# Kernel optimization log

Hardware: AMD Instinct MI355X
Metric: run time of the kernel (lower is better)

The kernel has to match this reference:

```python
import jax, jax.numpy as jnp
import numpy as np
import math

T_SCALE = 99
FEAT_DIM = 400
BATCH = 2
C = 256
NH = 8
NS = 32
NSPB = 3
RATIO = 0.5
LOCAL_STEP = 33


def build_sample_mask(T=T_SCALE, ns=NS, nspb=NSPB, ratio=RATIO):
    # Vectorized port of _get_interp1d_mask. Flat layout: [time, (bin, start, end)].
    N = ns * nspb
    e_idx, s_idx = np.meshgrid(np.arange(T), np.arange(T), indexing='ij')
    valid = s_idx < e_idx
    starts_i = s_idx[valid].astype(np.int64)
    ends_i = e_idx[valid].astype(np.int64)
    starts = starts_i.astype(np.float64)
    ends = ends_i.astype(np.float64)
    center = ends - starts + 1.0
    xmin = starts - center * ratio
    plen = (ends + center * ratio) - xmin
    S = xmin[:, None] + (plen / (N - 1.0))[:, None] * np.arange(N)[None, :]  # [P, N]
    down = np.trunc(S).astype(np.int64)  # matches int(math.modf(s)[1]) (trunc toward 0)
    dec = S - down                       # can be negative when s < 0, as in the original
    up = np.ceil(S).astype(np.int64)
    bin_col = (np.arange(N) // nspb)[None, :] * (T * T) + (starts_i * T + ends_i)[:, None]
    M = np.zeros(T * ns * T * T, np.float64)
    vd = (down >= 0) & (down <= T - 1)
    np.add.at(M, (down * (ns * T * T) + bin_col)[vd], ((1.0 - dec) / nspb)[vd])
    vu = (up >= 0) & (up <= T - 1)
    np.add.at(M, (up * (ns * T * T) + bin_col)[vu], (dec / nspb)[vu])
    return M.reshape(T, ns * T * T).astype(np.float32)


def pos_ebb(scale, size):
    pos = jnp.arange(scale, dtype=jnp.float32)[:, None]
    div = jnp.exp(jnp.arange(0, size, 2, dtype=jnp.float32) * (-math.log(10000.0) / size))
    ang = pos * div
    # interleave sin (even) / cos (odd)
    return jnp.stack([jnp.sin(ang), jnp.cos(ang)], axis=-1).reshape(scale, size)


def layer_norm(x, g, b, eps=1e-5):
    mu = jnp.mean(x, -1, keepdims=True)
    var = jnp.mean((x - mu) ** 2, -1, keepdims=True)
    return (x - mu) * jax.lax.rsqrt(var + eps) * g + b


def mha(x, w_qkv, b_qkv, w_o, b_o, nh=NH):
    t, b, c = x.shape
    hd = c // nh
    q, k, v = jnp.split(x @ w_qkv.T + b_qkv, 3, axis=-1)
    q = q.reshape(t, b, nh, hd)
    k = k.reshape(t, b, nh, hd)
    v = v.reshape(t, b, nh, hd)
    att = jnp.einsum('qbhd,kbhd->bhqk', q, k) / math.sqrt(hd)
    att = jax.nn.softmax(att, axis=-1)
    o = jnp.einsum('bhqk,kbhd->qbhd', att, v).reshape(t, b, c)
    return o @ w_o.T + b_o


def encoder(x, p):
    # PyTorch post-norm TransformerEncoder (eval mode, dropout off) + final LayerNorm
    (qkv_w, qkv_b, o_w, o_b, l1_w, l1_b, l2_w, l2_b, n1_g, n1_b, n2_g, n2_b, nf_g, nf_b) = p
    for i in range(qkv_w.shape[0]):
        a = mha(x, qkv_w[i], qkv_b[i], o_w[i], o_b[i])
        x = layer_norm(x + a, n1_g[i], n1_b[i])
        f = jax.nn.relu(x @ l1_w[i].T + l1_b[i]) @ l2_w[i].T + l2_b[i]
        x = layer_norm(x + f, n2_g[i], n2_b[i])
    return layer_norm(x, nf_g, nf_b)


def conv1d(x, w, b, pad, groups=1):
    y = jax.lax.conv_general_dilated(x, w, (1,), [(pad, pad)],
                                     dimension_numbers=('NCH', 'OIH', 'NCH'),
                                     feature_group_count=groups)
    return y + b[None, :, None]


def conv2d(x, w, b, pad):
    y = jax.lax.conv_general_dilated(x, w, (1, 1), [(pad, pad), (pad, pad)],
                                     dimension_numbers=('NCHW', 'OIHW', 'NCHW'))
    return y + b[None, :, None, None]


def conv3d(x, w, b, stride):
    y = jax.lax.conv_general_dilated(x, w, stride, [(0, 0)] * 3,
                                     dimension_numbers=('NCDHW', 'OIDHW', 'NCDHW'))
    return y + b[None, :, None, None, None]


def _forward(x, cb_w, cb_b, tg_qkv_w, tg_qkv_b, tg_o_w, tg_o_b, tg_l1_w, tg_l1_b, tg_l2_w, tg_l2_b, tg_n1_g, tg_n1_b, tg_n2_g, tg_n2_b, tg_nf_g, tg_nf_b, tl_qkv_w, tl_qkv_b, tl_o_w, tl_o_b, tl_l1_w, tl_l1_b, tl_l2_w, tl_l2_b, tl_n1_g, tl_n1_b, tl_n2_g, tl_n2_b, tl_nf_g, tl_nf_b, s1_w, s1_b, s2_w, s2_b, c3_w, c3_b, p1_w, p1_b, p2_w, p2_b, p3_w, p3_b, sample_mask):
    B, _, T = x.shape
    base = jax.nn.relu(conv1d(x, cb_w, cb_b, pad=1, groups=4))  # [B,C,T]
    # local transformer on LOCAL_STEP-strided windows
    group = T // LOCAL_STEP
    tl_p = (tl_qkv_w, tl_qkv_b, tl_o_w, tl_o_b, tl_l1_w, tl_l1_b, tl_l2_w, tl_l2_b, tl_n1_g, tl_n1_b, tl_n2_g, tl_n2_b, tl_nf_g, tl_nf_b)
    feat = base.reshape(B, C, LOCAL_STEP, group).transpose(2, 3, 0, 1).reshape(LOCAL_STEP, B * group, C)
    feat = encoder(feat + pos_ebb(LOCAL_STEP, C)[:, None, :], tl_p)
    local = feat.reshape(LOCAL_STEP * group, B, C).transpose(1, 2, 0)  # [B,C,T]
    # global bidirectional transformer (shared weights, flipped second pass)
    tg_p = (tg_qkv_w, tg_qkv_b, tg_o_w, tg_o_b, tg_l1_w, tg_l1_b, tg_l2_w, tg_l2_b, tg_n1_g, tg_n1_b, tg_n2_g, tg_n2_b, tg_nf_g, tg_nf_b)
    g = base.transpose(2, 0, 1)  # [T,B,C]
    pe = pos_ebb(T, C)[:, None, :]
    f1 = encoder(g + pe, tg_p)
    f2 = encoder(g[::-1] + pe, tg_p)
    base2 = local + (f1 + f2[::-1]).transpose(1, 2, 0)  # [B,C,T]
    s = jax.nn.relu(conv1d(base2, s1_w, s1_b, pad=1, groups=4))
    start1 = jax.nn.sigmoid(conv1d(s, s2_w, s2_b, pad=0))[:, 0, :]  # [B,T]
    # boundary-matching layer: dense matmul against precomputed interp mask
    bm = jnp.matmul(base2, sample_mask).reshape(B, C, NS, T, T)
    p = jax.nn.relu(conv3d(bm, c3_w, c3_b, (NS, 1, 1)))[:, :, 0]  # [B,C,T,T]
    p = jax.nn.relu(conv2d(p, p1_w, p1_b, pad=1))
    p = jax.nn.relu(conv2d(p, p2_w, p2_b, pad=1))
    cm = jax.nn.sigmoid(conv2d(p, p3_w, p3_b, pad=0))  # [B,2,T,T]
    return cm, start1


def setup_inputs() -> dict:
    key = jax.random.key(0)
    ks = iter(jax.random.split(key, 80))
    def rnd(shape):
        return 0.02 * jax.random.normal(next(ks), shape, dtype=jnp.float32)
    inp = {'x': jax.random.normal(next(ks), (BATCH, FEAT_DIM, T_SCALE), dtype=jnp.float32)}
    inp['cb_w'] = rnd((C, FEAT_DIM // 4, 3)); inp['cb_b'] = jnp.zeros((C,), jnp.float32)
    for pre, n in (('tg', 6), ('tl', 3)):
        inp[pre + '_qkv_w'] = rnd((n, 3 * C, C)); inp[pre + '_qkv_b'] = jnp.zeros((n, 3 * C), jnp.float32)
        inp[pre + '_o_w'] = rnd((n, C, C)); inp[pre + '_o_b'] = jnp.zeros((n, C), jnp.float32)
        inp[pre + '_l1_w'] = rnd((n, 1024, C)); inp[pre + '_l1_b'] = jnp.zeros((n, 1024), jnp.float32)
        inp[pre + '_l2_w'] = rnd((n, C, 1024)); inp[pre + '_l2_b'] = jnp.zeros((n, C), jnp.float32)
        inp[pre + '_n1_g'] = jnp.ones((n, C), jnp.float32); inp[pre + '_n1_b'] = jnp.zeros((n, C), jnp.float32)
        inp[pre + '_n2_g'] = jnp.ones((n, C), jnp.float32); inp[pre + '_n2_b'] = jnp.zeros((n, C), jnp.float32)
        inp[pre + '_nf_g'] = jnp.ones((C,), jnp.float32); inp[pre + '_nf_b'] = jnp.zeros((C,), jnp.float32)
    inp['s1_w'] = rnd((C, C // 4, 3)); inp['s1_b'] = jnp.zeros((C,), jnp.float32)
    inp['s2_w'] = rnd((1, C, 1)); inp['s2_b'] = jnp.zeros((1,), jnp.float32)
    inp['c3_w'] = rnd((C, C, NS, 1, 1)); inp['c3_b'] = jnp.zeros((C,), jnp.float32)
    inp['p1_w'] = rnd((C, C, 3, 3)); inp['p1_b'] = jnp.zeros((C,), jnp.float32)
    inp['p2_w'] = rnd((C, C, 3, 3)); inp['p2_b'] = jnp.zeros((C,), jnp.float32)
    inp['p3_w'] = rnd((2, C, 1, 1)); inp['p3_b'] = jnp.zeros((2,), jnp.float32)
    inp['sample_mask'] = jnp.asarray(build_sample_mask())  # [T, NS*T*T], exact BMN interp mask
    return inp


def reference(x, cb_w, cb_b, tg_qkv_w, tg_qkv_b, tg_o_w, tg_o_b, tg_l1_w, tg_l1_b, tg_l2_w, tg_l2_b, tg_n1_g, tg_n1_b, tg_n2_g, tg_n2_b, tg_nf_g, tg_nf_b, tl_qkv_w, tl_qkv_b, tl_o_w, tl_o_b, tl_l1_w, tl_l1_b, tl_l2_w, tl_l2_b, tl_n1_g, tl_n1_b, tl_n2_g, tl_n2_b, tl_nf_g, tl_nf_b, s1_w, s1_b, s2_w, s2_b, c3_w, c3_b, p1_w, p1_b, p2_w, p2_b, p3_w, p3_b, sample_mask):
    return _forward(x, cb_w, cb_b, tg_qkv_w, tg_qkv_b, tg_o_w, tg_o_b, tg_l1_w, tg_l1_b, tg_l2_w, tg_l2_b, tg_n1_g, tg_n1_b, tg_n2_g, tg_n2_b, tg_nf_g, tg_nf_b, tl_qkv_w, tl_qkv_b, tl_o_w, tl_o_b, tl_l1_w, tl_l1_b, tl_l2_w, tl_l2_b, tl_n1_g, tl_n1_b, tl_n2_g, tl_n2_b, tl_nf_g, tl_nf_b, s1_w, s1_b, s2_w, s2_b, c3_w, c3_b, p1_w, p1_b, p2_w, p2_b, p3_w, p3_b, sample_mask)
```

## Files before the change

kernel.cpp:

```cpp
#include <hip/hip_runtime.h>
#include <math.h>

#define T99   99
#define CC    256
#define NHH   8
#define FEAT  400
#define NS_   32
#define LSTEP 33

typedef __attribute__((ext_vector_type(8))) short s8v;
typedef __attribute__((ext_vector_type(4))) float f4v;

__device__ __forceinline__ void mfma_bf16(f4v& d, s8v a, s8v b) {
  asm volatile("v_mfma_f32_16x16x32_bf16 %0, %1, %2, %0" : "+v"(d) : "v"(a), "v"(b));
}

__device__ __forceinline__ unsigned short f2bf(float f) {
  union { float f; unsigned u; } x; x.f = f;
  unsigned r = x.u + 0x7FFFu + ((x.u >> 16) & 1u);
  return (unsigned short)(r >> 16);
}
__device__ __forceinline__ float bf2f(unsigned short h) {
  union { unsigned u; float f; } x; x.u = ((unsigned)h) << 16;
  return x.f;
}
__device__ __forceinline__ float blo(unsigned u) { union { unsigned x; float f; } c; c.x = u << 16; return c.f; }
__device__ __forceinline__ float bhi(unsigned u) { union { unsigned x; float f; } c; c.x = u & 0xffff0000u; return c.f; }

__device__ __forceinline__ float pe_val(int pos, int c) {
  int i = c >> 1;
  float freq = expf((float)(2 * i) * (-0.03597789207803197f));
  float ang = (float)pos * freq;
  return (c & 1) ? cosf(ang) : sinf(ang);
}

__global__ __launch_bounds__(128) void k_convbase(const float* __restrict__ x,
                                                  const float* __restrict__ w,
                                                  const float* __restrict__ bias,
                                                  float* __restrict__ base) {
  int b = blockIdx.x >> 8, co = blockIdx.x & 255, t = threadIdx.x;
  if (t >= T99) return;
  int g = co >> 6;
  float acc = bias[co];
  const float* xp = x + (size_t)(b * FEAT + g * 100) * T99;
  const float* wp = w + (size_t)co * 300;
  for (int ic = 0; ic < 100; ++ic) {
    float x0 = (t > 0)  ? xp[ic * T99 + t - 1] : 0.f;
    float x1 = xp[ic * T99 + t];
    float x2 = (t < 98) ? xp[ic * T99 + t + 1] : 0.f;
    acc += wp[ic * 3] * x0 + wp[ic * 3 + 1] * x1 + wp[ic * 3 + 2] * x2;
  }
  base[(size_t)(b * CC + co) * T99 + t] = fmaxf(acc, 0.f);
}

__global__ __launch_bounds__(256) void k_convW(const float* __restrict__ qkv, const float* __restrict__ o,
                                               const float* __restrict__ l1, const float* __restrict__ l2,
                                               int L, unsigned short* __restrict__ dst) {
  int total = L * 786432;
  for (int idx = blockIdx.x * 256 + threadIdx.x; idx < total; idx += gridDim.x * 256) {
    int l = idx / 786432, r = idx % 786432;
    float v;
    if (r < 196608)      v = qkv[(size_t)l * 196608 + r];
    else if (r < 262144) v = o[(size_t)l * 65536 + (r - 196608)];
    else if (r < 524288) v = l1[(size_t)l * 262144 + (r - 262144)];
    else                 v = l2[(size_t)l * 262144 + (r - 524288)];
    dst[idx] = f2bf(v);
  }
}

__global__ __launch_bounds__(256) void k_build_xg(const float* __restrict__ base, float* __restrict__ xg,
                                                  unsigned short* __restrict__ xgb) {
  int idx = blockIdx.x * 256 + threadIdx.x;
  int t = idx >> 10, r = idx & 1023, b4 = r >> 8, c = r & 255;
  float v = (b4 < 2) ? base[(size_t)(b4 * CC + c) * T99 + t]
                     : base[(size_t)((b4 - 2) * CC + c) * T99 + (98 - t)];
  v += pe_val(t, c);
  xg[idx] = v; xgb[idx] = f2bf(v);
}

__global__ __launch_bounds__(256) void k_build_xl(const float* __restrict__ base, float* __restrict__ xl,
                                                  unsigned short* __restrict__ xlb) {
  int idx = blockIdx.x * 256 + threadIdx.x;
  int ls = idx / 1536, r = idx % 1536, j = r >> 8, c = r & 255;
  int g = j >> 1, b = j & 1, t = ls * 3 + g;
  float v = base[(size_t)(b * CC + c) * T99 + t] + pe_val(ls, c);
  xl[idx] = v; xlb[idx] = f2bf(v);
}

__device__ __forceinline__ void gemm_body(const unsigned short* __restrict__ A,
                                          const unsigned short* __restrict__ W,
                                          const float* __restrict__ bias,
                                          const float* __restrict__ R,
                                          float* __restrict__ Y,
                                          unsigned short* __restrict__ Yb,
                                          int M, int N, int K, int flags,
                                          int m0, int n0) {
  __shared__ __align__(16) unsigned short Al[64][40];
  __shared__ __align__(16) unsigned short Bl[64][40];
  int tid = threadIdx.x;
  int lane = tid & 63, w = tid >> 6, wm = w >> 1, wn = w & 1;
  int sp = tid >> 2, kc = (tid & 3) << 3;
  f4v zero4 = {0.f, 0.f, 0.f, 0.f};
  f4v acc[2][2];
#pragma unroll
  for (int mt = 0; mt < 2; ++mt)
#pragma unroll
    for (int nt = 0; nt < 2; ++nt) acc[mt][nt] = zero4;

  for (int k0 = 0; k0 < K; k0 += 32) {
    s8v av = {0, 0, 0, 0, 0, 0, 0, 0};
    int row = m0 + sp;
    if (row < M) av = *(const s8v*)&A[(size_t)row * K + k0 + kc];
    *(s8v*)&Al[sp][kc] = av;
    *(s8v*)&Bl[sp][kc] = *(const s8v*)&W[(size_t)(n0 + sp) * K + k0 + kc];
    __syncthreads();
    s8v af[2], bf[2];
#pragma unroll
    for (int mt = 0; mt < 2; ++mt)
      af[mt] = *(const s8v*)&Al[wm * 32 + mt * 16 + (lane & 15)][(lane >> 4) * 8];
#pragma unroll
    for (int nt = 0; nt < 2; ++nt)
      bf[nt] = *(const s8v*)&Bl[wn * 32 + nt * 16 + (lane & 15)][(lane >> 4) * 8];
#pragma unroll
    for (int mt = 0; mt < 2; ++mt)
#pragma unroll
      for (int nt = 0; nt < 2; ++nt) mfma_bf16(acc[mt][nt], af[mt], bf[nt]);
    __syncthreads();
  }
  asm volatile("s_nop 7\n\ts_nop 7\n\ts_nop 4");
#pragma unroll
  for (int mt = 0; mt < 2; ++mt) {
#pragma unroll
    for (int nt = 0; nt < 2; ++nt) {
      int col = n0 + wn * 32 + nt * 16 + (lane & 15);
      float bv = bias[col];
#pragma unroll
      for (int r = 0; r < 2 * 2; ++r) {
        int row = m0 + wm * 32 + mt * 16 + (lane >> 4) * 4 + r;
        if (row < M) {
          float v = acc[mt][nt][r] + bv;
          if (flags & 2) v += R[(size_t)row * N + col];
          if (flags & 1) v = fmaxf(v, 0.f);
          if (!(flags & 8)) Y[(size_t)row * N + col] = v;
          if (flags & 4) Yb[(size_t)row * N + col] = f2bf(v);
        }
      }
    }
  }
}

__global__ __launch_bounds__(256) void k_gemmb(const unsigned short* __restrict__ A,
                                               const unsigned short* __restrict__ W,
                                               const float* __restrict__ bias,
                                               const float* __restrict__ R,
                                               float* __restrict__ Y,
                                               unsigned short* __restrict__ Yb,
                                               int M, int N, int K, int flags) {
  gemm_body(A, W, bias, R, Y, Yb, M, N, K, flags, blockIdx.x * 64, blockIdx.y * 64);
}

__global__ __launch_bounds__(256) void k_gemmb2(const unsigned short* __restrict__ A0,
                                                const unsigned short* __restrict__ W0,
                                                const float* __restrict__ bias0,
                                                const float* __restrict__ R0,
                                                float* __restrict__ Y0,
                                                unsigned short* __restrict__ Yb0,
                                                int M0,
                                                const unsigned short* __restrict__ A1,
                                                const unsigned short* __restrict__ W1,
                                                const float* __restrict__ bias1,
                                                const float* __restrict__ R1,
                                                float* __restrict__ Y1,
                                                unsigned short* __restrict__ Yb1,
                                                int M1,
                                                int N, int K, int flags) {
  int m0 = blockIdx.x * 64;
  if (blockIdx.z == 0) {
    if (m0 >= M0) return;
    gemm_body(A0, W0, bias0, R0, Y0, Yb0, M0, N, K, flags, m0, blockIdx.y * 64);
  } else {
    if (m0 >= M1) return;
    gemm_body(A1, W1, bias1, R1, Y1, Yb1, M1, N, K, flags, m0, blockIdx.y * 64);
  }
}

__device__ __forceinline__ void attn_body(const unsigned short* __restrict__ qkv,
                                          unsigned short* __restrict__ attb,
                                          int T_, int B_, int bid) {
  __shared__ float qv[32];
  __shared__ float red[128];
  __shared__ float pv[128];
  int tid = threadIdx.x;
  int q = bid % T_;
  int h = (bid / T_) % NHH;
  int b = bid / (T_ * NHH);
  if (tid < 32) qv[tid] = bf2f(qkv[(size_t)(q * B_ + b) * 768 + h * 32 + tid]);
  __syncthreads();
  float s = -1e30f;
  if (tid < T_) {
    const unsigned short* kp = qkv + (size_t)(tid * B_ + b) * 768 + 256 + h * 32;
    float d = 0;
#pragma unroll
    for (int i = 0; i < 32; ++i) d += qv[i] * bf2f(kp[i]);
    s = d * 0.176776695296636881f;
  }
  red[tid] = s; __syncthreads();
  for (int o = 64; o > 0; o >>= 1) { if (tid < o) red[tid] = fmaxf(red[tid], red[tid + o]); __syncthreads(); }
  float mx = red[0]; __syncthreads();
  float p = (tid < T_) ? expf(s - mx) : 0.f;
  pv[tid] = p; red[tid] = p; __syncthreads();
  for (int o = 64; o > 0; o >>= 1) { if (tid < o) red[tid] += red[tid + o]; __syncthreads(); }
  float denom = red[0];
  if (tid < 32) {
    float o = 0;
    for (int k = 0; k < T_; ++k) o += pv[k] * bf2f(qkv[(size_t)(k * B_ + b) * 768 + 512 + h * 32 + tid]);
    attb[(size_t)(q * B_ + b) * 256 + h * 32 + tid] = f2bf(o / denom);
  }
}

__global__ __launch_bounds__(128) void k_attn(const unsigned short* __restrict__ qkv,
                                              unsigned short* __restrict__ attb,
                                              int T_, int B_) {
  attn_body(qkv, attb, T_, B_, blockIdx.x);
}

__global__ __launch_bounds__(128) void k_attn2(const unsigned short* __restrict__ qkv0,
                                               unsigned short* __restrict__ attb0, int T0, int B0,
                                               const unsigned short* __restrict__ qkv1,
                                               unsigned short* __restrict__ attb1, int T1, int B1) {
  int bid = blockIdx.x;
  if (blockIdx.z == 0) {
    if (bid >= B0 * NHH * T0) return;
    attn_body(qkv0, attb0, T0, B0, bid);
  } else {
    if (bid >= B1 * NHH * T1) return;
    attn_body(qkv1, attb1, T1, B1, bid);
  }
}

__device__ __forceinline__ void ln_body(const float* __restrict__ X, const float* __restrict__ g,
                                        const float* __restrict__ bb, float* __restrict__ Y,
                                        unsigned short* __restrict__ Yb, int tok) {
  __shared__ float rs[256], rq[256];
  int c = threadIdx.x;
  float v = X[(size_t)tok * 256 + c];
  rs[c] = v; rq[c] = v * v; __syncthreads();
  for (int o = 128; o > 0; o >>= 1) { if (c < o) { rs[c] += rs[c + o]; rq[c] += rq[c + o]; } __syncthreads(); }
  float mu = rs[0] * (1.f / 256.f);
  float var = rq[0] * (1.f / 256.f) - mu * mu;
  float r = (v - mu) * rsqrtf(var + 1e-5f) * g[c] + bb[c];
  Y[(size_t)tok * 256 + c] = r;
  if (Yb) Yb[(size_t)tok * 256 + c] = f2bf(r);
}

__global__ __launch_bounds__(256) void k_ln(const float* __restrict__ X, const float* __restrict__ g,
                                            const float* __restrict__ bb, float* __restrict__ Y,
                                            unsigned short* __restrict__ Yb) {
  ln_body(X, g, bb, Y, Yb, blockIdx.x);
}

__global__ __launch_bounds__(256) void k_ln2(const float* __restrict__ X0, const float* __restrict__ g0,
                                             const float* __restrict__ bb0, float* __restrict__ Y0,
                                             unsigned short* __restrict__ Yb0, int n0,
                                             const float* __restrict__ X1, const float* __restrict__ g1,
                                             const float* __restrict__ bb1, float* __restrict__ Y1,
                                             unsigned short* __restrict__ Yb1, int n1) {
  int tok = blockIdx.x;
  if (blockIdx.z == 0) {
    if (tok >= n0) return;
    ln_body(X0, g0, bb0, Y0, Yb0, tok);
  } else {
    if (tok >= n1) return;
    ln_body(X1, g1, bb1, Y1, Yb1, tok);
  }
}

__global__ __launch_bounds__(256) void k_combine(const float* __restrict__ encl, const float* __restrict__ encg,
                                                 float* __restrict__ base2) {
  int idx = blockIdx.x * 256 + threadIdx.x;
  int t = idx % T99, c = (idx / T99) & 255, b = idx / (CC * T99);
  int ls = t / 3, g = t % 3;
  float v = encl[(size_t)(ls * 6 + g * 2 + b) * 256 + c]
          + encg[(size_t)(t * 4 + b) * 256 + c]
          + encg[(size_t)((98 - t) * 4 + 2 + b) * 256 + c];
  base2[idx] = v;
}

__global__ __launch_bounds__(128) void k_s1(const float* __restrict__ base2, const float* __restrict__ w,
                                            const float* __restrict__ bias, float* __restrict__ sbuf) {
  int b = blockIdx.x >> 8, co = blockIdx.x & 255, t = threadIdx.x;
  if (t >= T99) return;
  int g = co >> 6;
  float acc = bias[co];
  const float* xp = base2 + (size_t)(b * CC + g * 64) * T99;
  const float* wp = w + (size_t)co * 192;
  for (int ic = 0; ic < 64; ++ic) {
    float x0 = (t > 0)  ? xp[ic * T99 + t - 1] : 0.f;
    float x1 = xp[ic * T99 + t];
    float x2 = (t < 98) ? xp[ic * T99 + t + 1] : 0.f;
    acc += wp[ic * 3] * x0 + wp[ic * 3 + 1] * x1 + wp[ic * 3 + 2] * x2;
  }
  sbuf[(size_t)(b * CC + co) * T99 + t] = fmaxf(acc, 0.f);
}

__global__ __launch_bounds__(256) void k_s2(const float* __restrict__ sbuf, const float* __restrict__ w,
                                            const float* __restrict__ bias, float* __restrict__ out) {
  __shared__ float rs[256];
  int b = blockIdx.x / T99, t = blockIdx.x % T99, c = threadIdx.x;
  rs[c] = w[c] * sbuf[(size_t)(b * CC + c) * T99 + t];
  __syncthreads();
  for (int o = 128; o > 0; o >>= 1) { if (c < o) rs[c] += rs[c + o]; __syncthreads(); }
  if (c == 0) out[blockIdx.x] = 1.f / (1.f + expf(-(rs[0] + bias[0])));
}

__global__ __launch_bounds__(256) void k_w3t(const float* __restrict__ c3w, float* __restrict__ w3t) {
  int idx = blockIdx.x * 256 + threadIdx.x;
  int co = idx & 255, ci = (idx >> 8) & 255, n = idx >> 16;
  w3t[idx] = c3w[((size_t)(co << 8) + ci) * 32 + n];
}

__global__ __launch_bounds__(256) void k_G(const float* __restrict__ w3t, const float* __restrict__ base2,
                                           unsigned short* __restrict__ Gb) {
  int tc = blockIdx.x, n = blockIdx.y, b = blockIdx.z;
  int co = threadIdx.x;
  int t0 = tc * 25;
  float acc[25];
#pragma unroll
  for (int q = 0; q < 25; ++q) acc[q] = 0.f;
  const float* w = w3t + (size_t)n * 65536 + co;
  const float* bs = base2 + (size_t)b * CC * T99 + t0;
  for (int ci = 0; ci < 256; ++ci) {
    float wv = w[(size_t)ci * 256];
#pragma unroll
    for (int q = 0; q < 25; ++q) acc[q] += wv * bs[ci * T99 + q];
  }
#pragma unroll
  for (int q = 0; q < 25; ++q) {
    int t = t0 + q;
    if (t < T99) Gb[((size_t)(n * T99 + t) * 256 + co) * 2 + b] = f2bf(acc[q]);
  }
  if (tc == 0 && n == 0 && b == 0)
    ((unsigned int*)(Gb + (size_t)NS_ * T99 * 512))[co] = 0u;
}

__global__ __launch_bounds__(128) void k_ppre(const unsigned short* __restrict__ Gb,
                                              const float* __restrict__ c3b,
                                              unsigned int* __restrict__ pinb32) {
  __shared__ float w0s[96], w1s[96];
  __shared__ int   ofs[96];
  int e = blockIdx.x % T99, s = blockIdx.x / T99;
  int tid = threadIdx.x;
  if (s >= e) {
    float z0 = fmaxf(c3b[2 * tid], 0.f), z1 = fmaxf(c3b[2 * tid + 1], 0.f);
    unsigned int zz = ((unsigned)f2bf(z1) << 16) | (unsigned)f2bf(z0);
    pinb32[((size_t)(0 * T99 + s) * T99 + e) * 128 + tid] = zz;
    pinb32[((size_t)(1 * T99 + s) * T99 + e) * 128 + tid] = zz;
    return;
  }
  if (tid < 96) {
    double center = (double)(e - s + 1);
    double S = ((double)s - 0.5 * center) + ((2.0 * center - 1.0) / 95.0) * (double)tid;
    double dn = trunc(S);
    double dec = S - dn;
    int di = (int)dn;
    double uc = ceil(S);
    int ui = (int)uc;
    int n = tid / 3;
    float w0 = 0.f, w1 = 0.f;
    int r0 = 0;
    if (dn >= 0.0 && dn <= 98.0) {
      r0 = di;
      w0 = (float)((1.0 - dec) / 3.0);
      if (uc >= 0.0 && uc <= 98.0) {
        if (ui == di) w0 += (float)(dec / 3.0);
        else          w1  = (float)(dec / 3.0);
      }
    }
    w0s[tid] = w0; w1s[tid] = w1;
    ofs[tid] = (n * T99 + r0) * 1024;
  }
  __syncthreads();
  float a00 = 0.f, a01 = 0.f, a10 = 0.f, a11 = 0.f;
  const char* basep = (const char*)Gb + tid * 8;
#pragma unroll 8
  for (int k = 0; k < 96; ++k) {
    float w0 = w0s[k], w1 = w1s[k];
    const uint2* p = (const uint2*)(basep + ofs[k]);
    uint2 u0 = p[0];
    uint2 u1 = p[128];
    a00 += w0 * blo(u0.x) + w1 * blo(u1.x);
    a01 += w0 * bhi(u0.x) + w1 * bhi(u1.x);
    a10 += w0 * blo(u0.y) + w1 * blo(u1.y);
    a11 += w0 * bhi(u0.y) + w1 * bhi(u1.y);
  }
  float b0 = c3b[2 * tid], b1 = c3b[2 * tid + 1];
  unsigned int zb0 = ((unsigned)f2bf(fmaxf(a10 + b1, 0.f)) << 16) | (unsigned)f2bf(fmaxf(a00 + b0, 0.f));
  unsigned int zb1 = ((unsigned)f2bf(fmaxf(a11 + b1, 0.f)) << 16) | (unsigned)f2bf(fmaxf(a01 + b0, 0.f));
  pinb32[((size_t)(0 * T99 + s) * T99 + e) * 128 + tid] = zb0;
  pinb32[((size_t)(1 * T99 + s) * T99 + e) * 128 + tid] = zb1;
}

__global__ __launch_bounds__(256) void k_wb2(const float* __restrict__ pw, unsigned short* __restrict__ wb2) {
  int idx = blockIdx.x * 256 + threadIdx.x;
  int ci = idx & 255, co = (idx >> 8) & 255, tap = idx >> 16;
  wb2[idx] = f2bf(pw[((size_t)(co << 8) + ci) * 9 + tap]);
}

__global__ __launch_bounds__(256) void k_conv3x3(const unsigned short* __restrict__ in,
                                                 const unsigned short* __restrict__ wb2,
                                                 const float* __restrict__ bias,
                                                 unsigned short* __restrict__ out) {
  __shared__ __align__(16) unsigned short Al[128][40];
  __shared__ __align__(16) unsigned short Bl[128][40];
  int b = blockIdx.z;
  int co0 = blockIdx.y * 128;
  int ti = blockIdx.x / 13, tj = blockIdx.x % 13;
  int i0 = ti * 16, j0 = tj * 8;
  int tid = threadIdx.x;
  int lane = tid & 63, w = tid >> 6;
  int wm = w >> 1, wn = w & 1;

  f4v zero4 = {0.f, 0.f, 0.f, 0.f};
  f4v acc[4][4];
#pragma unroll
  for (int mt = 0; mt < 4; ++mt)
#pragma unroll
    for (int nt = 0; nt < 4; ++nt) acc[mt][nt] = zero4;

  for (int step = 0; step < 72; ++step) {
    int tap = step >> 3;
    int di = tap / 3 - 1, dj = tap % 3 - 1;
    int c0 = (step & 7) * 32;
#pragma unroll
    for (int h = 0; h < 2; ++h) {
      int v = tid + h * 256;
      int sp = v >> 2, kc = (v & 3) << 3;
      int gi = i0 + (sp >> 3) + di;
      int gj = j0 + (sp & 7) + dj;
      s8v val = {0, 0, 0, 0, 0, 0, 0, 0};
      if (gi >= 0 && gi < T99 && gj >= 0 && gj < T99)
        val = *(const s8v*)&in[((size_t)(b * T99 + gi) * T99 + gj) * 256 + c0 + kc];
      *(s8v*)&Al[sp][kc] = val;
      *(s8v*)&Bl[sp][kc] = *(const s8v*)&wb2[((size_t)tap * 256 + (co0 + sp)) * 256 + c0 + kc];
    }
    __syncthreads();
    s8v af[4], bf[4];
#pragma unroll
    for (int mt = 0; mt < 4; ++mt)
      af[mt] = *(const s8v*)&Al[wm * 64 + mt * 16 + (lane & 15)][(lane >> 4) * 8];
#pragma unroll
    for (int nt = 0; nt < 4; ++nt)
      bf[nt] = *(const s8v*)&Bl[wn * 64 + nt * 16 + (lane & 15)][(lane >> 4) * 8];
#pragma unroll
    for (int mt = 0; mt < 4; ++mt)
#pragma unroll
      for (int nt = 0; nt < 4; ++nt) mfma_bf16(acc[mt][nt], af[mt], bf[nt]);
    __syncthreads();
  }
  asm volatile("s_nop 7\n\ts_nop 7\n\ts_nop 4");
#pragma unroll
  for (int mt = 0; mt < 4; ++mt) {
#pragma unroll
    for (int nt = 0; nt < 4; ++nt) {
      int coL = wn * 64 + nt * 16 + (lane & 15);
      int co = co0 + coL;
      float bv = bias[co];
#pragma unroll
      for (int r = 0; r < 4; ++r) {
        int sp = wm * 64 + mt * 16 + (lane >> 4) * 4 + r;
        int gi = i0 + (sp >> 3), gj = j0 + (sp & 7);
        if (gi < T99 && gj < T99) {
          float v = acc[mt][nt][r] + bv;
          v = fmaxf(v, 0.f);
          out[((size_t)(b * T99 + gi) * T99 + gj) * 256 + co] = f2bf(v);
        }
      }
    }
  }
}

__global__ __launch_bounds__(256) void k_p3(const unsigned short* __restrict__ p2o,
                                            const float* __restrict__ w, const float* __restrict__ bias,
                                            float* __restrict__ cm) {
  int idx = blockIdx.x * 256 + threadIdx.x;
  if (idx >= 2 * 2 * T99 * T99) return;
  int j = idx % T99, i = (idx / T99) % T99, c2 = (idx / (T99 * T99)) % 2, b = idx / (2 * T99 * T99);
  float acc = bias[c2];
  const unsigned short* row = p2o + ((size_t)(b * T99 + i) * T99 + j) * 256;
  const float* wr = w + c2 * 256;
  for (int c8 = 0; c8 < 256; c8 += 8) {
    s8v v = *(const s8v*)&row[c8];
#pragma unroll
    for (int q = 0; q < 8; ++q) acc += wr[c8 + q] * bf2f((unsigned short)v[q]);
  }
  cm[idx] = 1.f / (1.f + expf(-acc));
}

struct EncW {
  const float *qkvw, *qkvb, *ow, *ob, *l1w, *l1b, *l2w, *l2b, *n1g, *n1b, *n2g, *n2b, *nfg, *nfb;
};

static void enc_layer(float* X, unsigned short* Xb, int ntok, int l,
                      const EncW& W, const unsigned short* Wb,
                      unsigned short* qkvbb, unsigned short* attb, float* yb,
                      int T_, int B_, hipStream_t st) {
  int mg = (ntok + 63) / 64;
  const unsigned short* wq = Wb + (size_t)l * 786432;
  k_gemmb<<<dim3(mg, 12), dim3(256), 0, st>>>(Xb, wq, W.qkvb + l * 768, nullptr, nullptr, qkvbb,
                                              ntok, 768, 256, 4 | 8);
  k_attn<<<dim3(B_ * NHH * T_), dim3(128), 0, st>>>(qkvbb, attb, T_, B_);
  k_gemmb<<<dim3(mg, 4), dim3(256), 0, st>>>(attb, wq + 196608, W.ob + l * 256, X, yb, nullptr,
                                             ntok, 256, 256, 2);
  k_ln<<<dim3(ntok), dim3(256), 0, st>>>(yb, W.n1g + l * 256, W.n1b + l * 256, X, Xb);
  k_gemmb<<<dim3(mg, 16), dim3(256), 0, st>>>(Xb, wq + 262144, W.l1b + l * 1024, nullptr, nullptr, qkvbb,
                                              ntok, 1024, 256, 1 | 4 | 8);
  k_gemmb<<<dim3(mg, 4), dim3(256), 0, st>>>(qkvbb, wq + 524288, W.l2b + l * 256, X, yb, nullptr,
                                             ntok, 256, 1024, 2);
  k_ln<<<dim3(ntok), dim3(256), 0, st>>>(yb, W.n2g + l * 256, W.n2b + l * 256, X, Xb);
}

extern "C" void kernel_launch(void* const* d_in, const int* in_sizes, int n_in,
                              void* d_out, int out_size, void* d_ws, size_t ws_size,
                              hipStream_t stream) {
  (void)in_sizes; (void)n_in; (void)out_size; (void)ws_size;
  const float* x    = (const float*)d_in[0];
  const float* cbw  = (const float*)d_in[1];
  const float* cbb  = (const float*)d_in[2];
  EncW tg = {(const float*)d_in[3],  (const float*)d_in[4],  (const float*)d_in[5],  (const float*)d_in[6],
             (const float*)d_in[7],  (const float*)d_in[8],  (const float*)d_in[9],  (const float*)d_in[10],
             (const float*)d_in[11], (const float*)d_in[12], (const float*)d_in[13], (const float*)d_in[14],
             (const float*)d_in[15], (const float*)d_in[16]};
  EncW tl = {(const float*)d_in[17], (const float*)d_in[18], (const float*)d_in[19], (const float*)d_in[20],
             (const float*)d_in[21], (const float*)d_in[22], (const float*)d_in[23], (const float*)d_in[24],
             (const float*)d_in[25], (const float*)d_in[26], (const float*)d_in[27], (const float*)d_in[28],
             (const float*)d_in[29], (const float*)d_in[30]};
  const float* s1w = (const float*)d_in[31];
  const float* s1b = (const float*)d_in[32];
  const float* s2w = (const float*)d_in[33];
  const float* s2b = (const float*)d_in[34];
  const float* c3w = (const float*)d_in[35];
  const float* c3b = (const float*)d_in[36];
  const float* p1w = (const float*)d_in[37];
  const float* p1b = (const float*)d_in[38];
  const float* p2w = (const float*)d_in[39];
  const float* p2b = (const float*)d_in[40];
  const float* p3w = (const float*)d_in[41];
  const float* p3b = (const float*)d_in[42];

  float* outp = (float*)d_out;

  char* wp = (char*)d_ws;
  auto alloc = [&](size_t bytes) -> void* {
    void* p = (void*)wp;
    wp += (bytes + 255) & ~(size_t)255;
    return p;
  };
  float* base  = (float*)alloc(sizeof(float) * 2 * CC * T99);
  float* xg    = (float*)alloc(sizeof(float) * T99 * 4 * CC);
  float* xl    = (float*)alloc(sizeof(float) * LSTEP * 6 * CC);
  unsigned short* xgb = (unsigned short*)alloc(sizeof(short) * T99 * 4 * CC);
  unsigned short* xlb = (unsigned short*)alloc(sizeof(short) * LSTEP * 6 * CC);
  unsigned short* qkvbbG = (unsigned short*)alloc(sizeof(short) * 396 * 1024);
  unsigned short* qkvbbL = (unsigned short*)alloc(sizeof(short) * 198 * 1024);
  unsigned short* attbG  = (unsigned short*)alloc(sizeof(short) * 396 * 256);
  unsigned short* attbL  = (unsigned short*)alloc(sizeof(short) * 198 * 256);
  float* ybG   = (float*)alloc(sizeof(float) * 396 * 256);
  float* ybL   = (float*)alloc(sizeof(float) * 198 * 256);
  float* encg  = (float*)alloc(sizeof(float) * T99 * 4 * CC);
  float* encl  = (float*)alloc(sizeof(float) * LSTEP * 6 * CC);
  float* base2 = (float*)alloc(sizeof(float) * 2 * CC * T99);
  float* sbuf  = (float*)alloc(sizeof(float) * 2 * CC * T99);
  float* w3t   = (float*)alloc(sizeof(float) * 32 * 256 * 256);
  unsigned short* Gb = (unsigned short*)alloc(sizeof(short) * (2 * NS_ * T99 * 256 + 512));
  unsigned short* pinb = (unsigned short*)alloc(sizeof(short) * 2 * T99 * T99 * 256);
  unsigned short* p1o  = (unsigned short*)alloc(sizeof(short) * 2 * T99 * T99 * 256);
  unsigned short* p2o  = (unsigned short*)alloc(sizeof(short) * 2 * T99 * T99 * 256);
  unsigned short* wb2a = (unsigned short*)alloc(sizeof(short) * 9 * 256 * 256);
  unsigned short* wb2b = (unsigned short*)alloc(sizeof(short) * 9 * 256 * 256);
  unsigned short* wtgb = (unsigned short*)alloc(sizeof(short) * 6 * 786432);
  unsigned short* wtlb = (unsigned short*)alloc(sizeof(short) * 3 * 786432);

  k_convW<<<dim3(4096), dim3(256), 0, stream>>>(tg.qkvw, tg.ow, tg.l1w, tg.l2w, 6, wtgb);
  k_convW<<<dim3(2048), dim3(256), 0, stream>>>(tl.qkvw, tl.ow, tl.l1w, tl.l2w, 3, wtlb);
  k_w3t<<<dim3(8192), dim3(256), 0, stream>>>(c3w, w3t);
  k_wb2<<<dim3(2304), dim3(256), 0, stream>>>(p1w, wb2a);
  k_wb2<<<dim3(2304), dim3(256), 0, stream>>>(p2w, wb2b);
  k_convbase<<<dim3(512), dim3(128), 0, stream>>>(x, cbw, cbb, base);
  k_build_xl<<<dim3(198), dim3(256), 0, stream>>>(base, xl, xlb);
  k_build_xg<<<dim3(396), dim3(256), 0, stream>>>(base, xg, xgb);

  const int ML = 198, MG = 396;
  const int mgL = 4, mgG = 7;
  for (int l = 0; l < 3; ++l) {
    const unsigned short* wqL = wtlb + (size_t)l * 786432;
    const unsigned short* wqG = wtgb + (size_t)l * 786432;
    k_gemmb2<<<dim3(mgG, 12, 2), dim3(256), 0, stream>>>(
        xlb, wqL, tl.qkvb + l * 768, nullptr, nullptr, qkvbbL, ML,
        xgb, wqG, tg.qkvb + l * 768, nullptr, nullptr, qkvbbG, MG, 768, 256, 4 | 8);
    k_attn2<<<dim3(4 * NHH * T99, 1, 2), dim3(128), 0, stream>>>(
        qkvbbL, attbL, LSTEP, 6, qkvbbG, attbG, T99, 4);
    k_gemmb2<<<dim3(mgG, 4, 2), dim3(256), 0, stream>>>(
        attbL, wqL + 196608, tl.ob + l * 256, xl, ybL, nullptr, ML,
        attbG, wqG + 196608, tg.ob + l * 256, xg, ybG, nullptr, MG, 256, 256, 2);
    k_ln2<<<dim3(MG, 1, 2), dim3(256), 0, stream>>>(
        ybL, tl.n1g + l * 256, tl.n1b + l * 256, xl, xlb, ML,
        ybG, tg.n1g + l * 256, tg.n1b + l * 256, xg, xgb, MG);
    k_gemmb2<<<dim3(mgG, 16, 2), dim3(256), 0, stream>>>(
        xlb, wqL + 262144, tl.l1b + l * 1024, nullptr, nullptr, qkvbbL, ML,
        xgb, wqG + 262144, tg.l1b + l * 1024, nullptr, nullptr, qkvbbG, MG, 1024, 256, 1 | 4 | 8);
    k_gemmb2<<<dim3(mgG, 4, 2), dim3(256), 0, stream>>>(
        qkvbbL, wqL + 524288, tl.l2b + l * 256, xl, ybL, nullptr, ML,
        qkvbbG, wqG + 524288, tg.l2b + l * 256, xg, ybG, nullptr, MG, 256, 1024, 2);
    k_ln2<<<dim3(MG, 1, 2), dim3(256), 0, stream>>>(
        ybL, tl.n2g + l * 256, tl.n2b + l * 256, xl, xlb, ML,
        ybG, tg.n2g + l * 256, tg.n2b + l * 256, xg, xgb, MG);
  }
  for (int l = 3; l < 6; ++l)
    enc_layer(xg, xgb, MG, l, tg, wtgb, qkvbbG, attbG, ybG, T99, 4, stream);
  k_ln2<<<dim3(MG, 1, 2), dim3(256), 0, stream>>>(
      xl, tl.nfg, tl.nfb, encl, nullptr, ML,
      xg, tg.nfg, tg.nfb, encg, nullptr, MG);
  k_combine<<<dim3(198), dim3(256), 0, stream>>>(encl, encg, base2);
  k_s1<<<dim3(512), dim3(128), 0, stream>>>(base2, s1w, s1b, sbuf);
  k_s2<<<dim3(198), dim3(256), 0, stream>>>(sbuf, s2w, s2b, outp + 2 * 2 * T99 * T99);
  k_G<<<dim3(4, 32, 2), dim3(256), 0, stream>>>(w3t, base2, Gb);
  k_ppre<<<dim3(T99 * T99), dim3(128), 0, stream>>>(Gb, c3b, (unsigned int*)pinb);
  k_conv3x3<<<dim3(91, 2, 2), dim3(256), 0, stream>>>(pinb, wb2a, p1b, p1o);
  k_conv3x3<<<dim3(91, 2, 2), dim3(256), 0, stream>>>(p1o, wb2b, p2b, p2o);
  k_p3<<<dim3(154), dim3(256), 0, stream>>>(p2o, p3w, p3b, outp);
}
```

Measured before the change: 724.9 us.

## Stage halo input tile once in LDS and stream prepacked weights from global

The 3x3 conv kernel now loads a 10x10 spatial halo tile with all 256 input channels into shared memory once, instead of reloading per tap and channel slice. It reads weights straight from global memory in a layout prepacked to match the MFMA fragment order. Output tiles shrink to 8x8 (169 blocks per plane), and the 72 per-step barriers are removed. In exchange the kernel uses about 52KB of LDS per block, which may limit occupancy, and every wave re-reads weights from global/L2.

New measurement: 759.6 us. 1.05x slower.

```diff
diff --git a/kernel.cpp b/kernel.cpp
--- a/kernel.cpp
+++ b/kernel.cpp
@@ -400,78 +400,91 @@
   pinb32[((size_t)(1 * T99 + s) * T99 + e) * 128 + tid] = zb1;
 }
 
-__global__ __launch_bounds__(256) void k_wb2(const float* __restrict__ pw, unsigned short* __restrict__ wb2) {
+__global__ __launch_bounds__(256) void k_wb2(const float* __restrict__ pw, unsigned short* __restrict__ wbf) {
   int idx = blockIdx.x * 256 + threadIdx.x;
-  int ci = idx & 255, co = (idx >> 8) & 255, tap = idx >> 16;
-  wb2[idx] = f2bf(pw[((size_t)(co << 8) + ci) * 9 + tap]);
+  if (idx >= 73728) return;
+  int lane = idx & 63;
+  int cog  = (idx >> 6) & 15;
+  int kst  = (idx >> 10) & 7;
+  int tap  = idx >> 13;
+  int co = cog * 16 + (lane & 15);
+  int k  = kst * 32 + (lane >> 4) * 8;
+  s8v v;
+#pragma unroll
+  for (int j = 0; j < 8; ++j)
+    v[j] = (short)f2bf(pw[((size_t)co * 256 + k + j) * 9 + tap]);
+  *(s8v*)&wbf[(size_t)idx * 8] = v;
 }
 
 __global__ __launch_bounds__(256) void k_conv3x3(const unsigned short* __restrict__ in,
-                                                 const unsigned short* __restrict__ wb2,
+                                                 const unsigned short* __restrict__ wbf,
                                                  const float* __restrict__ bias,
                                                  unsigned short* __restrict__ out) {
-  __shared__ __align__(16) unsigned short Al[128][40];
-  __shared__ __align__(16) unsigned short Bl[128][40];
+  __shared__ __align__(16) unsigned short Ah[100 * 264];
   int b = blockIdx.z;
   int co0 = blockIdx.y * 128;
   int ti = blockIdx.x / 13, tj = blockIdx.x % 13;
-  int i0 = ti * 16, j0 = tj * 8;
+  int i0 = ti * 8, j0 = tj * 8;
   int tid = threadIdx.x;
-  int lane = tid & 63, w = tid >> 6;
-  int wm = w >> 1, wn = w & 1;
-
-  f4v zero4 = {0.f, 0.f, 0.f, 0.f};
-  f4v acc[4][4];
-#pragma unroll
-  for (int mt = 0; mt < 4; ++mt)
-#pragma unroll
-    for (int nt = 0; nt < 4; ++nt) acc[mt][nt] = zero4;
-
-  for (int step = 0; step < 72; ++step) {
-    int tap = step >> 3;
-    int di = tap / 3 - 1, dj = tap % 3 - 1;
-    int c0 = (step & 7) * 32;
-#pragma unroll
-    for (int h = 0; h < 2; ++h) {
-      int v = tid + h * 256;
-      int sp = v >> 2, kc = (v & 3) << 3;
-      int gi = i0 + (sp >> 3) + di;
-      int gj = j0 + (sp & 7) + dj;
+#pragma unroll
+  for (int it = 0; it < 13; ++it) {
+    int chunk = it * 256 + tid;
+    if (chunk < 3200) {
+      int row = chunk >> 5;
+      int cc = (chunk & 31) * 8;
+      int gi = i0 + row / 10 - 1, gj = j0 + row % 10 - 1;
       s8v val = {0, 0, 0, 0, 0, 0, 0, 0};
       if (gi >= 0 && gi < T99 && gj >= 0 && gj < T99)
-        val = *(const s8v*)&in[((size_t)(b * T99 + gi) * T99 + gj) * 256 + c0 + kc];
-      *(s8v*)&Al[sp][kc] = val;
-      *(s8v*)&Bl[sp][kc] = *(const s8v*)&wb2[((size_t)tap * 256 + (co0 + sp)) * 256 + c0 + kc];
+        val = *(const s8v*)&in[((size_t)(b * T99 + gi) * T99 + gj) * 256 + cc];
+      *(s8v*)&Ah[row * 264 + cc] = val;
     }
-    __syncthreads();
-    s8v af[4], bf[4];
-#pragma unroll
-    for (int mt = 0; mt < 4; ++mt)
-      af[mt] = *(const s8v*)&Al[wm * 64 + mt * 16 + (lane & 15)][(lane >> 4) * 8];
-#pragma unroll
-    for (int nt = 0; nt < 4; ++nt)
-      bf[nt] = *(const s8v*)&Bl[wn * 64 + nt * 16 + (lane & 15)][(lane >> 4) * 8];
-#pragma unroll
-    for (int mt = 0; mt < 4; ++mt)
-#pragma unroll
-      for (int nt = 0; nt < 4; ++nt) mfma_bf16(acc[mt][nt], af[mt], bf[nt]);
-    __syncthreads();
+  }
+  __syncthreads();
+
+  int lane = tid & 63, w = tid >> 6, wm = w >> 1, wn = w & 1;
+  int l15 = lane & 15, lk = lane >> 4;
+  int spL0 = wm * 32 + l15;
+  int spL1 = spL0 + 16;
+  int hr0 = (spL0 >> 3) * 10 + (spL0 & 7) + 11;
+  int hr1 = (spL1 >> 3) * 10 + (spL1 & 7) + 11;
+  int cogbase = blockIdx.y * 8 + wn * 4;
+
+  f4v acc[2][4];
+#pragma unroll
+  for (int mt = 0; mt < 2; ++mt)
+#pragma unroll
+    for (int nt = 0; nt < 4; ++nt) acc[mt][nt] = (f4v){0.f, 0.f, 0.f, 0.f};
+
+  for (int tap = 0; tap < 9; ++tap) {
+    int doff = (tap / 3) * 10 + (tap % 3) - 11;
+    const unsigned short* bbase = wbf + ((size_t)(tap * 8) * 16) * 512 + (size_t)lane * 8;
+#pragma unroll
+    for (int kst = 0; kst < 8; ++kst) {
+      int k0 = kst * 32;
+      s8v a0 = *(const s8v*)&Ah[(hr0 + doff) * 264 + k0 + lk * 8];
+      s8v a1 = *(const s8v*)&Ah[(hr1 + doff) * 264 + k0 + lk * 8];
+      const unsigned short* bp = bbase + ((size_t)(kst * 16 + cogbase)) * 512;
+#pragma unroll
+      for (int nt = 0; nt < 4; ++nt) {
+        s8v bf = *(const s8v*)&bp[(size_t)nt * 512];
+        mfma_bf16(acc[0][nt], a0, bf);
+        mfma_bf16(acc[1][nt], a1, bf);
+      }
+    }
   }
   asm volatile("s_nop 7\n\ts_nop 7\n\ts_nop 4");
 #pragma unroll
-  for (int mt = 0; mt < 4; ++mt) {
+  for (int mt = 0; mt < 2; ++mt) {
 #pragma unroll
     for (int nt = 0; nt < 4; ++nt) {
-      int coL = wn * 64 + nt * 16 + (lane & 15);
-      int co = co0 + coL;
+      int co = co0 + wn * 64 + nt * 16 + l15;
       float bv = bias[co];
 #pragma unroll
       for (int r = 0; r < 4; ++r) {
-        int sp = wm * 64 + mt * 16 + (lane >> 4) * 4 + r;
+        int sp = wm * 32 + mt * 16 + lk * 4 + r;
         int gi = i0 + (sp >> 3), gj = j0 + (sp & 7);
         if (gi < T99 && gj < T99) {
-          float v = acc[mt][nt][r] + bv;
-          v = fmaxf(v, 0.f);
+          float v = fmaxf(acc[mt][nt][r] + bv, 0.f);
           out[((size_t)(b * T99 + gi) * T99 + gj) * 256 + co] = f2bf(v);
         }
       }
@@ -583,14 +596,14 @@
   k_convW<<<dim3(4096), dim3(256), 0, stream>>>(tg.qkvw, tg.ow, tg.l1w, tg.l2w, 6, wtgb);
   k_convW<<<dim3(2048), dim3(256), 0, stream>>>(tl.qkvw, tl.ow, tl.l1w, tl.l2w, 3, wtlb);
   k_w3t<<<dim3(8192), dim3(256), 0, stream>>>(c3w, w3t);
-  k_wb2<<<dim3(2304), dim3(256), 0, stream>>>(p1w, wb2a);
-  k_wb2<<<dim3(2304), dim3(256), 0, stream>>>(p2w, wb2b);
+  k_wb2<<<dim3(288), dim3(256), 0, stream>>>(p1w, wb2a);
+  k_wb2<<<dim3(288), dim3(256), 0, stream>>>(p2w, wb2b);
   k_convbase<<<dim3(512), dim3(128), 0, stream>>>(x, cbw, cbb, base);
   k_build_xl<<<dim3(198), dim3(256), 0, stream>>>(base, xl, xlb);
   k_build_xg<<<dim3(396), dim3(256), 0, stream>>>(base, xg, xgb);
 
   const int ML = 198, MG = 396;
-  const int mgL = 4, mgG = 7;
+  const int mgG = 7;
   for (int l = 0; l < 3; ++l) {
     const unsigned short* wqL = wtlb + (size_t)l * 786432;
     const unsigned short* wqG = wtgb + (size_t)l * 786432;
@@ -625,7 +638,7 @@
   k_s2<<<dim3(198), dim3(256), 0, stream>>>(sbuf, s2w, s2b, outp + 2 * 2 * T99 * T99);
   k_G<<<dim3(4, 32, 2), dim3(256), 0, stream>>>(w3t, base2, Gb);
   k_ppre<<<dim3(T99 * T99), dim3(128), 0, stream>>>(Gb, c3b, (unsigned int*)pinb);
-  k_conv3x3<<<dim3(91, 2, 2), dim3(256), 0, stream>>>(pinb, wb2a, p1b, p1o);
-  k_conv3x3<<<dim3(91, 2, 2), dim3(256), 0, stream>>>(p1o, wb2b, p2b, p2o);
+  k_conv3x3<<<dim3(169, 2, 2), dim3(256), 0, stream>>>(pinb, wb2a, p1b, p1o);
+  k_conv3x3<<<dim3(169, 2, 2), dim3(256), 0, stream>>>(p1o, wb2b, p2b, p2o);
   k_p3<<<dim3(154), dim3(256), 0, stream>>>(p2o, p3w, p3b, outp);
 }
```
